# Kernel optimization log

Hardware: AMD Instinct MI355X
Metric: run time of the kernel (lower is better)

Reference implementation:

```python
import jax, jax.numpy as jnp
import numpy as np

HEAD_DIM = 128
N_HEADS = 16
N_KV_HEADS = 4
THETA = 10000.0
EPS = 1e-6


def setup_inputs() -> dict:
    key = jax.random.key(0)
    k1, k2, k3 = jax.random.split(key, 3)
    B, S = 2, 2048
    xq = jax.random.normal(k1, (B, S, N_HEADS * HEAD_DIM), dtype=jnp.float32)
    xk = jax.random.normal(k2, (B, S, N_KV_HEADS * HEAD_DIM), dtype=jnp.float32)
    xv = jax.random.normal(k3, (B, S, N_KV_HEADS * HEAD_DIM), dtype=jnp.float32)
    return {"xq": xq, "xk": xk, "xv": xv}


def _rope(x):
    # x: [b, h, s, d]; half-split rotary (y1 = x1*cos + x2*sin, y2 = -x1*sin + x2*cos)
    d = x.shape[-1]
    s = x.shape[2]
    inv_freq = (1.0 / THETA) ** (jnp.arange(0, d, 2, dtype=jnp.float32) / d)
    t = jnp.arange(s, dtype=jnp.float32)
    freqs = t[:, None] * inv_freq[None, :]          # [s, d/2]
    cos = jnp.cos(freqs)[None, None]                 # [1,1,s,d/2]
    sin = jnp.sin(freqs)[None, None]
    x1, x2 = jnp.split(x, 2, axis=-1)
    y1 = x1 * cos + x2 * sin
    y2 = -x1 * sin + x2 * cos
    return jnp.concatenate([y1, y2], axis=-1).astype(x.dtype)


def reference(xq, xk, xv):
    B, S, _ = xq.shape
    # b s (h a) -> b h s a
    q = xq.reshape(B, S, N_HEADS, HEAD_DIM).transpose(0, 2, 1, 3)
    k = xk.reshape(B, S, N_KV_HEADS, HEAD_DIM).transpose(0, 2, 1, 3)
    v = xv.reshape(B, S, N_KV_HEADS, HEAD_DIM).transpose(0, 2, 1, 3)
    # qk-norm (L2 normalize last dim with eps clamp, like F.normalize)
    q = q / jnp.maximum(jnp.linalg.norm(q, axis=-1, keepdims=True), EPS)
    k = k / jnp.maximum(jnp.linalg.norm(k, axis=-1, keepdims=True), EPS)
    # RoPE
    q = _rope(q)
    k = _rope(k)
    # GQA: repeat kv heads to match q heads
    rep = N_HEADS // N_KV_HEADS
    k = jnp.repeat(k, rep, axis=1)
    v = jnp.repeat(v, rep, axis=1)
    scale = 1.0 / jnp.sqrt(jnp.asarray(HEAD_DIM, dtype=q.dtype))
    scores = jnp.einsum('bhqd,bhkd->bhqk', q, k) * scale
    causal = jnp.tril(jnp.ones((S, S), dtype=bool))
    scores = jnp.where(causal[None, None], scores, jnp.asarray(-jnp.inf, scores.dtype))
    probs = jax.nn.softmax(scores, axis=-1)
    out = jnp.einsum('bhqk,bhkd->bhqd', probs, v)
    # b h s a -> b s (h a)
    return out.transpose(0, 2, 1, 3).reshape(B, S, N_HEADS * HEAD_DIM)
```

## Files before the change

kernel.cpp:

```cpp
#include <hip/hip_runtime.h>
#include <hip/hip_bf16.h>
#include <stdint.h>

#define S_LEN 2048
#define NB    2
#define HQ    16
#define HKV   4
#define HD    128
#define KVB   64
#define QBW   32
#define QBB   128

typedef __bf16 bf16_t;
typedef __attribute__((ext_vector_type(4)))  __bf16 bf16x4;
typedef __attribute__((ext_vector_type(8)))  __bf16 bf16x8;
typedef __attribute__((ext_vector_type(4)))  float  f32x4;
typedef __attribute__((ext_vector_type(16))) float  f32x16;
typedef __attribute__((ext_vector_type(4)))  unsigned int u32x4;

#define NVBLK 512

__constant__ int kOrder24[24] = {7,22,23,20,21, 6,18,19,16,17, 5,14,15,12,13,
                                 4,10,11,8,9, 3, 2, 1, 0};

__device__ __forceinline__ void gload_lds16(const bf16_t* g, bf16_t* l) {
  __builtin_amdgcn_global_load_lds(
      (const __attribute__((address_space(1))) unsigned int*)g,
      (__attribute__((address_space(3))) unsigned int*)l, 16, 0, 0);
}
__device__ __forceinline__ uint32_t pack2(float lo, float hi) {
  uint32_t a = (uint32_t)__builtin_bit_cast(unsigned short, (bf16_t)lo);
  uint32_t b = (uint32_t)__builtin_bit_cast(unsigned short, (bf16_t)hi);
  return a | (b << 16);
}
__device__ __forceinline__ void plswap(uint32_t& x, uint32_t& y) {
  asm volatile("v_permlane32_swap_b32 %0, %1" : "+v"(x), "+v"(y));
}

__global__ void preproc_kernel(const float* __restrict__ xq,
                               const float* __restrict__ xk,
                               const float* __restrict__ xv,
                               bf16_t* __restrict__ Qr,
                               bf16_t* __restrict__ Kf,
                               bf16_t* __restrict__ Vf) {
  __shared__ bf16_t tile[HD][34];
  if (blockIdx.x < NVBLK) {
    const int bid = blockIdx.x;
    const int bh  = bid >> 6;
    const int r6  = bid & 63;
    const int sc  = r6 >> 1;
    const int j   = r6 & 1;
    const int b = bh >> 2, hh = bh & 3;
    const int d  = threadIdx.x & 127;
    const int s2 = threadIdx.x >> 7;
    const float* src = xv + (size_t)b * S_LEN * (HKV * HD) + hh * HD;
    #pragma unroll 4
    for (int it = 0; it < 16; ++it) {
      int sl = it * 2 + s2;
      int s  = sc * 64 + j * 32 + sl;
      tile[d][sl] = (bf16_t)src[(size_t)s * (HKV * HD) + d];
    }
    __syncthreads();
    bf16_t* dstb = Vf + ((size_t)bh * 32 + sc) * (HD * KVB);
    const int dd   = threadIdx.x >> 1;
    const int dt   = dd >> 5, r0v = dd & 31;
    #pragma unroll
    for (int i = 0; i < 2; ++i) {
      const int cl = (threadIdx.x & 1) * 2 + i;
      const int c  = j * 4 + cl;
      const int n  = (c >> 1) * 256 + dt * 64 + (c & 1) * 32 + r0v;
      *reinterpret_cast<bf16x8*>(dstb + n * 8) =
          *reinterpret_cast<const bf16x8*>(&tile[dd][cl * 8]);
    }
    return;
  }
  int wid  = ((blockIdx.x - NVBLK) * blockDim.x + threadIdx.x) >> 6;
  int lane = threadIdx.x & 63;
  const int per_bs = HQ + HKV;
  int b   = wid / (S_LEN * per_bs);
  int rem = wid - b * (S_LEN * per_bs);
  int s   = rem / per_bs;
  int hh  = rem - s * per_bs;
  const float* src;
  float scale;
  if (hh < HQ) {
    src = xq + ((size_t)(b * S_LEN + s) * (HQ * HD)) + hh * HD;
    scale = 0.08838834764831845f * 1.4426950408889634f;
  } else {
    src = xk + ((size_t)(b * S_LEN + s) * (HKV * HD)) + (hh - HQ) * HD;
    scale = 1.0f;
  }
  float x1 = src[lane];
  float x2 = src[64 + lane];
  float ss = x1 * x1 + x2 * x2;
  #pragma unroll
  for (int mm = 1; mm < 64; mm <<= 1) ss += __shfl_xor(ss, mm, 64);
  float rinv = scale / fmaxf(sqrtf(ss), 1e-6f);
  float inv = exp2f(-(float)lane * 0.20762050593046938f);
  float ang = (float)s * inv;
  float cs = __cosf(ang), sn = __sinf(ang);
  float q1 = x1 * rinv, q2 = x2 * rinv;
  bf16_t y1 = (bf16_t)(q1 * cs + q2 * sn);
  bf16_t y2 = (bf16_t)(q2 * cs - q1 * sn);
  if (hh < HQ) {
    bf16_t* dst = Qr + (((size_t)(b * HQ + hh) * S_LEN + s) * HD);
    dst[lane]      = y1;
    dst[64 + lane] = y2;
  } else {
    bf16_t* dst = Kf + ((size_t)((b * HKV + (hh - HQ)) * 32 + (s >> 6))) * (KVB * HD);
    const int sl = s & 63, half = sl >> 5, r0k = sl & 31;
    const int kk = lane >> 4, hi = (lane >> 3) & 1, pos = lane & 7;
    const int a1 = (kk * 128 + half * 64 + hi * 32 + r0k) * 8 + pos;
    dst[a1]        = y1;
    dst[a1 + 4096] = y2;
  }
}

__global__ __launch_bounds__(256, 3)
void attn_kernel(const bf16_t* __restrict__ Qr,
                 const bf16_t* __restrict__ Kf,
                 const bf16_t* __restrict__ Vf,
                 float* __restrict__ out,
                 bf16_t* __restrict__ Opart,
                 float2* __restrict__ mlpart,
                 int split, int upb) {
  __shared__ bf16_t Kb[2][KVB * HD];
  __shared__ bf16_t Vb[HD * KVB];

  const int w    = threadIdx.x >> 6;
  const int lane = threadIdx.x & 63;
  const int r0   = lane & 31;
  const int hi   = lane >> 5;

  const int lid = (int)blockIdx.x;
  const int p   = lid & 7;
  const int qq  = lid >> 3;
  const int j   = qq & 3;
  const int k   = qq >> 2;
  const int b   = p >> 2;
  const int kvh = p & 3;
  const int h   = kvh * 4 + j;
  const int bh  = b * 16 + h;
  const int u   = split ? kOrder24[k] : (15 - k);
  int qt, t0, t1;
  if (!split || u < 8) {
    qt = u; t0 = 0; t1 = 2 * qt + 2;
  } else {
    int v = u - 8;
    qt = 8 + (v >> 1);
    int T = 2 * qt + 2, mid = qt + 1;
    if (v & 1) { t0 = mid; t1 = T; } else { t0 = 0; t1 = mid; }
  }
  const bool full = (t0 == 0) && (t1 == 2 * qt + 2);
  const int qw0  = qt * QBB + w * QBW;
  const int qrow = qw0 + r0;
  const int qmax = qw0 + 31;

  const bf16_t* Qbase = Qr + (size_t)(b * HQ  + h  ) * S_LEN * HD;
  const bf16_t* Kbase = Kf + (size_t)(b * HKV + kvh) * 32 * (KVB * HD);
  const bf16_t* Vbase = Vf + (size_t)(b * HKV + kvh) * 32 * (HD * KVB);

  const int soff = (w * 256 + lane) * 8;

  bf16x8 qf[8];
  #pragma unroll
  for (int kk = 0; kk < 8; ++kk)
    qf[kk] = *reinterpret_cast<const bf16x8*>(Qbase + (size_t)qrow * HD + kk * 16 + hi * 8);

  f32x16 accO[4];
  #pragma unroll
  for (int dt = 0; dt < 4; ++dt)
    #pragma unroll
    for (int e = 0; e < 16; ++e) accO[dt][e] = 0.f;
  float m = -3.0e38f, l = 0.f;

  {
    const bf16_t* kg = Kbase + (size_t)t0 * (KVB * HD);
    #pragma unroll
    for (int i = 0; i < 4; ++i)
      gload_lds16(kg + soff + i * 512, &Kb[0][soff + i * 512]);
  }

  for (int t = t0; t < t1; ++t) {
    const int pb = (t - t0) & 1;
    __builtin_amdgcn_s_barrier();
    {
      const bf16_t* vg = Vbase + (size_t)t * (HD * KVB);
      #pragma unroll
      for (int i = 0; i < 4; ++i)
        gload_lds16(vg + soff + i * 512, &Vb[soff + i * 512]);
      const int tn = (t + 1 < t1) ? t + 1 : t;
      const bf16_t* kg = Kbase + (size_t)tn * (KVB * HD);
      #pragma unroll
      for (int i = 0; i < 4; ++i)
        gload_lds16(kg + soff + i * 512, &Kb[pb ^ 1][soff + i * 512]);
    }
    asm volatile("s_waitcnt vmcnt(8)" ::: "memory");
    __builtin_amdgcn_sched_barrier(0);
    __builtin_amdgcn_s_barrier();
    __builtin_amdgcn_sched_barrier(0);

    const int kv0 = t * KVB;
    const bool active = (kv0 <= qmax);
    float p2[32];
    u32x4 pw[4];
    if (active) {
      const bf16_t* kb = &Kb[pb][0];
      f32x16 st0, st1;
      #pragma unroll
      for (int e = 0; e < 16; ++e) { st0[e] = 0.f; st1[e] = 0.f; }
      __builtin_amdgcn_s_setprio(1);
      #pragma unroll
      for (int kk = 0; kk < 8; ++kk) {
        bf16x8 k0 = *reinterpret_cast<const bf16x8*>(kb + kk * 1024 + lane * 8);
        bf16x8 k1 = *reinterpret_cast<const bf16x8*>(kb + kk * 1024 + 512 + lane * 8);
        st0 = __builtin_amdgcn_mfma_f32_32x32x16_bf16(k0, qf[kk], st0, 0, 0, 0);
        st1 = __builtin_amdgcn_mfma_f32_32x32x16_bf16(k1, qf[kk], st1, 0, 0, 0);
      }
      __builtin_amdgcn_s_setprio(0);

      const bool need_mask = (kv0 + 63 > qw0);
      #pragma unroll
      for (int jj = 0; jj < 2; ++jj)
        #pragma unroll
        for (int e = 0; e < 16; ++e) {
          float s = jj ? st1[e] : st0[e];
          if (need_mask) {
            int kv = kv0 + jj * 32 + (e & 3) + 8 * (e >> 2) + 4 * hi;
            s = (kv > qrow) ? -3.0e38f : s;
          }
          p2[jj * 16 + e] = s;
        }
      float mt[16];
      #pragma unroll
      for (int e = 0; e < 16; ++e) mt[e] = fmaxf(p2[e], p2[e + 16]);
      #pragma unroll
      for (int e = 0; e < 8; ++e) mt[e] = fmaxf(mt[e], mt[e + 8]);
      #pragma unroll
      for (int e = 0; e < 4; ++e) mt[e] = fmaxf(mt[e], mt[e + 4]);
      float lmx = fmaxf(fmaxf(mt[0], mt[1]), fmaxf(mt[2], mt[3]));
      float cmx = fmaxf(lmx, __shfl_xor(lmx, 32, 64));
      if (!__all(cmx <= m + 8.0f)) {
        float mnew = fmaxf(m, cmx);
        float resc = __builtin_amdgcn_exp2f(m - mnew);
        m = mnew;
        l *= resc;
        #pragma unroll
        for (int dt = 0; dt < 4; ++dt)
          #pragma unroll
          for (int e = 0; e < 16; ++e) accO[dt][e] *= resc;
      }
      #pragma unroll
      for (int e = 0; e < 32; ++e) p2[e] = __builtin_amdgcn_exp2f(p2[e] - m);
      float sv[16];
      #pragma unroll
      for (int e = 0; e < 16; ++e) sv[e] = p2[e] + p2[e + 16];
      #pragma unroll
      for (int e = 0; e < 8; ++e) sv[e] += sv[e + 8];
      #pragma unroll
      for (int e = 0; e < 4; ++e) sv[e] += sv[e + 4];
      float lsum = (sv[0] + sv[1]) + (sv[2] + sv[3]);
      l += lsum + __shfl_xor(lsum, 32, 64);

      #pragma unroll
      for (int jj = 0; jj < 2; ++jj) {
        const int o = jj * 16;
        {
          uint32_t A = pack2(p2[o + 0], p2[o + 1]);
          uint32_t C = pack2(p2[o + 2], p2[o + 3]);
          uint32_t B = pack2(p2[o + 4], p2[o + 5]);
          uint32_t D = pack2(p2[o + 6], p2[o + 7]);
          plswap(A, B);
          plswap(C, D);
          pw[2 * jj] = (u32x4){A, C, B, D};
        }
        {
          uint32_t A = pack2(p2[o + 8],  p2[o + 9]);
          uint32_t C = pack2(p2[o + 10], p2[o + 11]);
          uint32_t B = pack2(p2[o + 12], p2[o + 13]);
          uint32_t D = pack2(p2[o + 14], p2[o + 15]);
          plswap(A, B);
          plswap(C, D);
          pw[2 * jj + 1] = (u32x4){A, C, B, D};
        }
      }
    }

    asm volatile("s_waitcnt vmcnt(4)" ::: "memory");
    __builtin_amdgcn_sched_barrier(0);
    __builtin_amdgcn_s_barrier();
    __builtin_amdgcn_sched_barrier(0);

    if (active) {
      const bf16_t* vb = &Vb[0];
      __builtin_amdgcn_s_setprio(1);
      #pragma unroll
      for (int kk = 0; kk < 4; ++kk) {
        bf16x8 pf = __builtin_bit_cast(bf16x8, pw[kk]);
        #pragma unroll
        for (int dt = 0; dt < 4; ++dt) {
          bf16x8 vf = *reinterpret_cast<const bf16x8*>(vb + kk * 2048 + dt * 512 + lane * 8);
          accO[dt] = __builtin_amdgcn_mfma_f32_32x32x16_bf16(vf, pf, accO[dt], 0, 0, 0);
        }
      }
      __builtin_amdgcn_s_setprio(0);
    }
  }

  const float inv = 1.0f / l;
  if (full) {
    float* orow = out + ((size_t)(b * S_LEN + qrow) * (HQ * HD)) + h * HD + hi * 4;
    #pragma unroll
    for (int dt = 0; dt < 4; ++dt)
      #pragma unroll
      for (int rg = 0; rg < 4; ++rg) {
        f32x4 v4 = { accO[dt][4 * rg + 0] * inv, accO[dt][4 * rg + 1] * inv,
                     accO[dt][4 * rg + 2] * inv, accO[dt][4 * rg + 3] * inv };
        *reinterpret_cast<f32x4*>(orow + dt * 32 + rg * 8) = v4;
      }
  } else {
    const int c    = (t0 != 0) ? 1 : 0;
    const int pidx = ((bh << 3) + (qt - 8)) * 2 + c;
    bf16_t* Op = Opart + (size_t)pidx * (QBB * HD) + (size_t)(w * QBW + r0) * HD + hi * 4;
    #pragma unroll
    for (int dt = 0; dt < 4; ++dt)
      #pragma unroll
      for (int rg = 0; rg < 4; ++rg) {
        bf16x4 v4 = { (bf16_t)(accO[dt][4 * rg + 0] * inv),
                      (bf16_t)(accO[dt][4 * rg + 1] * inv),
                      (bf16_t)(accO[dt][4 * rg + 2] * inv),
                      (bf16_t)(accO[dt][4 * rg + 3] * inv) };
        *reinterpret_cast<bf16x4*>(Op + dt * 32 + rg * 8) = v4;
      }
    if (!hi) mlpart[(size_t)pidx * QBB + w * QBW + r0] = make_float2(m, l);
  }
}

__global__ void combine_kernel(const bf16_t* __restrict__ Opart,
                               const float2* __restrict__ mlpart,
                               float* __restrict__ out) {
  const int j  = blockIdx.x;
  const int bh = j >> 3;
  const int qt = 8 + (j & 7);
  const int b  = bh >> 4;
  const int h  = bh & 15;
  const int r  = threadIdx.x >> 1;
  const int d0 = (threadIdx.x & 1) * 64;
  const size_t pj0 = (size_t)(j * 2)     * (QBB * HD) + (size_t)r * HD + d0;
  const size_t pj1 = (size_t)(j * 2 + 1) * (QBB * HD) + (size_t)r * HD + d0;
  const float2 ml0 = mlpart[(size_t)(j * 2)     * QBB + r];
  const float2 ml1 = mlpart[(size_t)(j * 2 + 1) * QBB + r];
  const float M  = fmaxf(ml0.x, ml1.x);
  float b0 = exp2f(ml0.x - M) * ml0.y;
  float b1 = exp2f(ml1.x - M) * ml1.y;
  const float inv = 1.0f / (b0 + b1);
  b0 *= inv; b1 *= inv;
  const int qrow = qt * QBB + r;
  float* orow = out + ((size_t)(b * S_LEN + qrow) * (HQ * HD)) + h * HD + d0;
  #pragma unroll
  for (int i = 0; i < 8; ++i) {
    bf16x8 o0 = *reinterpret_cast<const bf16x8*>(Opart + pj0 + i * 8);
    bf16x8 o1 = *reinterpret_cast<const bf16x8*>(Opart + pj1 + i * 8);
    f32x4 lo = { b0 * (float)o0[0] + b1 * (float)o1[0],
                 b0 * (float)o0[1] + b1 * (float)o1[1],
                 b0 * (float)o0[2] + b1 * (float)o1[2],
                 b0 * (float)o0[3] + b1 * (float)o1[3] };
    f32x4 hi4 = { b0 * (float)o0[4] + b1 * (float)o1[4],
                  b0 * (float)o0[5] + b1 * (float)o1[5],
                  b0 * (float)o0[6] + b1 * (float)o1[6],
                  b0 * (float)o0[7] + b1 * (float)o1[7] };
    *reinterpret_cast<f32x4*>(orow + i * 8)     = lo;
    *reinterpret_cast<f32x4*>(orow + i * 8 + 4) = hi4;
  }
}

extern "C" void kernel_launch(void* const* d_in, const int* in_sizes, int n_in,
                              void* d_out, int out_size, void* d_ws, size_t ws_size,
                              hipStream_t stream) {
  const float* xq = (const float*)d_in[0];
  const float* xk = (const float*)d_in[1];
  const float* xv = (const float*)d_in[2];
  float* out = (float*)d_out;

  char* ws = (char*)d_ws;
  size_t off = 0;
  bf16_t* Qr = (bf16_t*)(ws + off); off += (size_t)NB * HQ  * S_LEN * HD * sizeof(bf16_t);
  bf16_t* Kf = (bf16_t*)(ws + off); off += (size_t)NB * HKV * S_LEN * HD * sizeof(bf16_t);
  bf16_t* Vf = (bf16_t*)(ws + off); off += (size_t)NB * HKV * S_LEN * HD * sizeof(bf16_t);
  bf16_t* Opart  = (bf16_t*)(ws + off); off += (size_t)512 * QBB * HD * sizeof(bf16_t);
  float2* mlpart = (float2*)(ws + off); off += (size_t)512 * QBB * sizeof(float2);
  const int split = (ws_size >= off) ? 1 : 0;
  const int upb   = split ? 24 : 16;

  const int nrow = NB * S_LEN * (HQ + HKV);
  preproc_kernel<<<NVBLK + nrow / 4, 256, 0, stream>>>(xq, xk, xv, Qr, Kf, Vf);

  attn_kernel<<<32 * upb, 256, 0, stream>>>(Qr, Kf, Vf, out, Opart, mlpart,
                                            split, upb);
  if (split)
    combine_kernel<<<256, 256, 0, stream>>>(Opart, mlpart, out);
}
```

Before: 91.87 us.

## Split long causal query tiles into up to four KV chunks for balance

Replaces the fixed two-way split of the upper eight query tiles with a table-driven split where query tiles 5-15 are divided into 2, 3 or 4 KV chunks depending on their length. Attention blocks grow from 768 to 1088, and combine_kernel merges up to four partials per row using the stored max and sum values. The goal is to even out per-block work and keep more CUs busy on the 256-CU MI355X. The cost is more partial-output traffic in bf16, a larger workspace, and a combine kernel with more blocks.

```diff
diff --git a/kernel.cpp b/kernel.cpp
--- a/kernel.cpp
+++ b/kernel.cpp
@@ -10,6 +10,7 @@
 #define KVB   64
 #define QBW   32
 #define QBB   128
+#define NSLOT 29
 
 typedef __bf16 bf16_t;
 typedef __attribute__((ext_vector_type(4)))  __bf16 bf16x4;
@@ -20,8 +21,19 @@
 
 #define NVBLK 512
 
-__constant__ int kOrder24[24] = {7,22,23,20,21, 6,18,19,16,17, 5,14,15,12,13,
-                                 4,10,11,8,9, 3, 2, 1, 0};
+__constant__ signed char kQt[34] = {15,15,15,15, 14,14,14, 13,13,13, 12,12,12,
+                                    11,11,11, 10,10,10, 9,9, 8,8, 7,7, 6,6,
+                                    5,5, 4, 3, 2, 1, 0};
+__constant__ signed char kC[34]  = { 0, 1, 2, 3,  0, 1, 2,  0, 1, 2,  0, 1, 2,
+                                     0, 1, 2,  0, 1, 2, 0,1, 0,1, 0,1, 0,1,
+                                     0,1, 0, 0, 0, 0, 0};
+
+__device__ __forceinline__ int nch_of(int qt) {
+  return (qt <= 4) ? 1 : (qt <= 9) ? 2 : (qt <= 14) ? 3 : 4;
+}
+__device__ __forceinline__ int pbase_of(int qt) {
+  return (qt <= 9) ? (qt - 5) * 2 : (qt <= 14) ? 10 + (qt - 10) * 3 : 25;
+}
 
 __device__ __forceinline__ void gload_lds16(const bf16_t* g, bf16_t* l) {
   __builtin_amdgcn_global_load_lds(
@@ -141,17 +153,19 @@
   const int kvh = p & 3;
   const int h   = kvh * 4 + j;
   const int bh  = b * 16 + h;
-  const int u   = split ? kOrder24[k] : (15 - k);
-  int qt, t0, t1;
-  if (!split || u < 8) {
-    qt = u; t0 = 0; t1 = 2 * qt + 2;
+  int qt, t0, t1, pidx = -1;
+  if (!split) {
+    qt = 15 - k; t0 = 0; t1 = 2 * qt + 2;
   } else {
-    int v = u - 8;
-    qt = 8 + (v >> 1);
-    int T = 2 * qt + 2, mid = qt + 1;
-    if (v & 1) { t0 = mid; t1 = T; } else { t0 = 0; t1 = mid; }
-  }
-  const bool full = (t0 == 0) && (t1 == 2 * qt + 2);
+    qt = kQt[k];
+    const int c   = kC[k];
+    const int nch = nch_of(qt);
+    const int T   = 2 * qt + 2;
+    t0 = c * T / nch;
+    t1 = (c + 1) * T / nch;
+    if (nch > 1) pidx = bh * NSLOT + pbase_of(qt) + c;
+  }
+  const bool full = (pidx < 0);
   const int qw0  = qt * QBB + w * QBW;
   const int qrow = qw0 + r0;
   const int qmax = qw0 + 31;
@@ -319,8 +333,6 @@
         *reinterpret_cast<f32x4*>(orow + dt * 32 + rg * 8) = v4;
       }
   } else {
-    const int c    = (t0 != 0) ? 1 : 0;
-    const int pidx = ((bh << 3) + (qt - 8)) * 2 + c;
     bf16_t* Op = Opart + (size_t)pidx * (QBB * HD) + (size_t)(w * QBW + r0) * HD + hi * 4;
     #pragma unroll
     for (int dt = 0; dt < 4; ++dt)
@@ -340,35 +352,48 @@
                                const float2* __restrict__ mlpart,
                                float* __restrict__ out) {
   const int j  = blockIdx.x;
-  const int bh = j >> 3;
-  const int qt = 8 + (j & 7);
+  const int bh = j / 11;
+  const int qt = 5 + (j % 11);
+  const int nch   = nch_of(qt);
+  const int slot0 = bh * NSLOT + pbase_of(qt);
   const int b  = bh >> 4;
   const int h  = bh & 15;
   const int r  = threadIdx.x >> 1;
   const int d0 = (threadIdx.x & 1) * 64;
-  const size_t pj0 = (size_t)(j * 2)     * (QBB * HD) + (size_t)r * HD + d0;
-  const size_t pj1 = (size_t)(j * 2 + 1) * (QBB * HD) + (size_t)r * HD + d0;
-  const float2 ml0 = mlpart[(size_t)(j * 2)     * QBB + r];
-  const float2 ml1 = mlpart[(size_t)(j * 2 + 1) * QBB + r];
-  const float M  = fmaxf(ml0.x, ml1.x);
-  float b0 = exp2f(ml0.x - M) * ml0.y;
-  float b1 = exp2f(ml1.x - M) * ml1.y;
-  const float inv = 1.0f / (b0 + b1);
-  b0 *= inv; b1 *= inv;
+  float wgt[4];
+  float M = -3.0e38f;
+  #pragma unroll
+  for (int c = 0; c < 4; ++c)
+    if (c < nch) {
+      float2 ml = mlpart[(size_t)(slot0 + c) * QBB + r];
+      wgt[c] = 0.f;
+      M = fmaxf(M, ml.x);
+    }
+  float wsum = 0.f;
+  #pragma unroll
+  for (int c = 0; c < 4; ++c)
+    if (c < nch) {
+      float2 ml = mlpart[(size_t)(slot0 + c) * QBB + r];
+      wgt[c] = exp2f(ml.x - M) * ml.y;
+      wsum += wgt[c];
+    }
+  const float inv = 1.0f / wsum;
   const int qrow = qt * QBB + r;
   float* orow = out + ((size_t)(b * S_LEN + qrow) * (HQ * HD)) + h * HD + d0;
   #pragma unroll
   for (int i = 0; i < 8; ++i) {
-    bf16x8 o0 = *reinterpret_cast<const bf16x8*>(Opart + pj0 + i * 8);
-    bf16x8 o1 = *reinterpret_cast<const bf16x8*>(Opart + pj1 + i * 8);
-    f32x4 lo = { b0 * (float)o0[0] + b1 * (float)o1[0],
-                 b0 * (float)o0[1] + b1 * (float)o1[1],
-                 b0 * (float)o0[2] + b1 * (float)o1[2],
-                 b0 * (float)o0[3] + b1 * (float)o1[3] };
-    f32x4 hi4 = { b0 * (float)o0[4] + b1 * (float)o1[4],
-                  b0 * (float)o0[5] + b1 * (float)o1[5],
-                  b0 * (float)o0[6] + b1 * (float)o1[6],
-                  b0 * (float)o0[7] + b1 * (float)o1[7] };
+    float acc[8] = {0.f, 0.f, 0.f, 0.f, 0.f, 0.f, 0.f, 0.f};
+    #pragma unroll
+    for (int c = 0; c < 4; ++c)
+      if (c < nch) {
+        const float wv = wgt[c] * inv;
+        bf16x8 o = *reinterpret_cast<const bf16x8*>(
+            Opart + (size_t)(slot0 + c) * (QBB * HD) + (size_t)r * HD + d0 + i * 8);
+        #pragma unroll
+        for (int e = 0; e < 8; ++e) acc[e] += wv * (float)o[e];
+      }
+    f32x4 lo = {acc[0], acc[1], acc[2], acc[3]};
+    f32x4 hi4 = {acc[4], acc[5], acc[6], acc[7]};
     *reinterpret_cast<f32x4*>(orow + i * 8)     = lo;
     *reinterpret_cast<f32x4*>(orow + i * 8 + 4) = hi4;
   }
@@ -387,10 +412,10 @@
   bf16_t* Qr = (bf16_t*)(ws + off); off += (size_t)NB * HQ  * S_LEN * HD * sizeof(bf16_t);
   bf16_t* Kf = (bf16_t*)(ws + off); off += (size_t)NB * HKV * S_LEN * HD * sizeof(bf16_t);
   bf16_t* Vf = (bf16_t*)(ws + off); off += (size_t)NB * HKV * S_LEN * HD * sizeof(bf16_t);
-  bf16_t* Opart  = (bf16_t*)(ws + off); off += (size_t)512 * QBB * HD * sizeof(bf16_t);
-  float2* mlpart = (float2*)(ws + off); off += (size_t)512 * QBB * sizeof(float2);
+  bf16_t* Opart  = (bf16_t*)(ws + off); off += (size_t)32 * NSLOT * QBB * HD * sizeof(bf16_t);
+  float2* mlpart = (float2*)(ws + off); off += (size_t)32 * NSLOT * QBB * sizeof(float2);
   const int split = (ws_size >= off) ? 1 : 0;
-  const int upb   = split ? 24 : 16;
+  const int upb   = split ? 34 : 16;
 
   const int nrow = NB * S_LEN * (HQ + HKV);
   preproc_kernel<<<NVBLK + nrow / 4, 256, 0, stream>>>(xq, xk, xv, Qr, Kf, Vf);
@@ -398,5 +423,5 @@
   attn_kernel<<<32 * upb, 256, 0, stream>>>(Qr, Kf, Vf, out, Opart, mlpart,
                                             split, upb);
   if (split)
-    combine_kernel<<<256, 256, 0, stream>>>(Opart, mlpart, out);
-}
+    combine_kernel<<<352, 256, 0, stream>>>(Opart, mlpart, out);
+}
```

Result: slower. 116.5 us (+26.8%).
